# Optimization experiments

Measured on AMD Instinct MI355X. Metric: run time of the kernel, lower is better.

The kernel has to match this reference:

```python
import jax, jax.numpy as jnp
import numpy as np

N, M, E, HID, H = 50000, 4000, 320000, 128, 2
EPS = 1e-5  # torch BatchNorm1d eps


def _lrelu(x):
    return jnp.where(x >= 0, x, 0.2 * x)


def _bn(x, g, b):
    # BatchNorm1d in training mode: biased batch statistics over dim 0
    m = x.mean(0)
    v = ((x - m) ** 2).mean(0)
    return g * (x - m) * jax.lax.rsqrt(v + EPS) + b


def _seg_softmax(a, idx, n):
    # softmax of a[E,heads] normalized per node index idx (PyG softmax)
    mx = jax.ops.segment_max(a, idx, num_segments=n)
    e = jnp.exp(a - mx[idx])
    s = jax.ops.segment_sum(e, idx, num_segments=n)
    return e / s[idx]


def _hgconv(x, he_n, he_e, he_w, W, att, bias, heads):
    # PyG HypergraphConv(use_attention=True, concat=False)
    xl = (x @ W).reshape(N, heads, HID)                  # lin(x) -> [N,heads,C]
    # hyperedge_attr = incidence^T @ x  (matches to_dense_adj path in HGAT)
    ea = jax.ops.segment_sum(x[he_n], he_e, num_segments=M)  # [M,F]
    eal = (ea @ W).reshape(M, heads, HID)                # lin(hyperedge_attr)
    a = (jnp.concatenate([xl[he_n], eal[he_e]], axis=-1) * att[0]).sum(-1)  # [E,heads]
    a = _seg_softmax(_lrelu(a), he_n, N)
    # degree normalizations
    Dn = jax.ops.segment_sum(he_w[he_e], he_n, num_segments=N)
    Dinv = jnp.where(Dn > 0, 1.0 / Dn, 0.0)
    Bn = jax.ops.segment_sum(jnp.ones((E,), x.dtype), he_e, num_segments=M)
    Binv = jnp.where(Bn > 0, 1.0 / Bn, 0.0)
    # node -> hyperedge
    m1 = Binv[he_e][:, None, None] * xl[he_n] * a[..., None]
    eo = jax.ops.segment_sum(m1, he_e, num_segments=M)   # [M,heads,C]
    # hyperedge -> node
    m2 = Dinv[he_n][:, None, None] * eo[he_e] * a[..., None]
    out = jax.ops.segment_sum(m2, he_n, num_segments=N)  # [N,heads,C]
    return out.mean(1) + bias                            # concat=False -> head mean


def _forward(x, he_w, lin1_w, lin1_b, bn1_g, bn1_b, h1_w, h1_att, h1_b,
             bn2_g, bn2_b, h2_w, h2_att, h2_b, bn3_g, bn3_b,
             lin2_w, lin2_b, bn4_g, bn4_b, he_n, he_e):
    src = x
    x = _bn(_lrelu(x @ lin1_w + lin1_b), bn1_g, bn1_b)
    x2 = _hgconv(x, he_n, he_e, he_w, h1_w, h1_att, h1_b, H)
    x = _bn(x + x2, bn2_g, bn2_b)
    x2 = _hgconv(x, he_n, he_e, he_w, h2_w, h2_att, h2_b, 1)
    x = _bn(x + x2, bn3_g, bn3_b)
    x = _lrelu(x @ lin2_w + lin2_b)
    return _bn(src + x, bn4_g, bn4_b)


def setup_inputs() -> dict:
    key = jax.random.key(0)
    ks = jax.random.split(key, 10)
    s = 0.05
    he_n = jax.random.randint(ks[0], (E,), 0, N, dtype=jnp.int32)
    he_e = (jnp.arange(E, dtype=jnp.int32) % M)  # every hyperedge id used
    return {
        'x': jax.random.normal(ks[1], (N, 128), jnp.float32),
        'he_n': he_n, 'he_e': he_e,
        'he_w': jnp.ones((M,), jnp.float32),
        'lin1_w': jax.random.normal(ks[2], (128, HID), jnp.float32) * s,
        'lin1_b': jnp.zeros((HID,), jnp.float32),
        'bn1_g': jnp.ones((HID,), jnp.float32), 'bn1_b': jnp.zeros((HID,), jnp.float32),
        'h1_w': jax.random.normal(ks[3], (HID, H * HID), jnp.float32) * s,
        'h1_att': jax.random.normal(ks[4], (1, H, 2 * HID), jnp.float32) * s,
        'h1_b': jnp.zeros((HID,), jnp.float32),
        'bn2_g': jnp.ones((HID,), jnp.float32), 'bn2_b': jnp.zeros((HID,), jnp.float32),
        'h2_w': jax.random.normal(ks[5], (HID, HID), jnp.float32) * s,
        'h2_att': jax.random.normal(ks[6], (1, 1, 2 * HID), jnp.float32) * s,
        'h2_b': jnp.zeros((HID,), jnp.float32),
        'bn3_g': jnp.ones((HID,), jnp.float32), 'bn3_b': jnp.zeros((HID,), jnp.float32),
        'lin2_w': jax.random.normal(ks[7], (HID, 128), jnp.float32) * s,
        'lin2_b': jnp.zeros((128,), jnp.float32),
        'bn4_g': jnp.ones((128,), jnp.float32), 'bn4_b': jnp.zeros((128,), jnp.float32),
    }


def reference(x, he_n, he_e, he_w, lin1_w, lin1_b, bn1_g, bn1_b, h1_w, h1_att, h1_b,
              bn2_g, bn2_b, h2_w, h2_att, h2_b, bn3_g, bn3_b,
              lin2_w, lin2_b, bn4_g, bn4_b):
    return _forward(x, he_w, lin1_w, lin1_b, bn1_g, bn1_b, h1_w, h1_att, h1_b,
                    bn2_g, bn2_b, h2_w, h2_att, h2_b, bn3_g, bn3_b,
                    lin2_w, lin2_b, bn4_g, bn4_b, he_n, he_e)
```

## Files before the change

### kernel.cpp

```cpp
#include <hip/hip_runtime.h>
#include <hip/hip_fp16.h>
#include <math.h>

constexpr int Nn = 50000;
constexpr int Mm = 4000;
constexpr int Ee = 320000;
constexpr int KPB = Ee / Mm;
constexpr float BINV = 1.0f / (float)KPB;
constexpr float EPSf = 1e-5f;
constexpr int NBKT = 16;
constexpr int NBSCAN = 49;

__device__ __forceinline__ float lrelu_f(float x) { return x >= 0.f ? x : 0.2f * x; }

__device__ __forceinline__ unsigned short f2h(float f) {
    __half h = __float2half_rn(f);
    return *reinterpret_cast<unsigned short*>(&h);
}
__device__ __forceinline__ float h2f(unsigned short s) {
    __half_raw r; r.x = s;
    return __half2float(__half(r));
}
__device__ __forceinline__ unsigned int packh2(float a, float b) {
    return (unsigned int)f2h(a) | ((unsigned int)f2h(b) << 16);
}
__device__ __forceinline__ float4 ldh4(const unsigned short* p) {
    ushort4 u = *(const ushort4*)p;
    return make_float4(h2f(u.x), h2f(u.y), h2f(u.z), h2f(u.w));
}
__device__ __forceinline__ float2 ldh2(const unsigned short* p) {
    ushort2 u = *(const ushort2*)p;
    return make_float2(h2f(u.x), h2f(u.y));
}

__device__ __forceinline__ float wave_sum(float v) {
#pragma unroll
    for (int o = 32; o >= 1; o >>= 1) v += __shfl_xor(v, o, 64);
    return v;
}

__device__ __forceinline__ void finalize_to_lds(const float* __restrict__ st,
                                                const float* __restrict__ g,
                                                const float* __restrict__ b,
                                                float* ABsh, int t) {
    if (t < 128) {
        double ds = 0, dq = 0;
#pragma unroll
        for (int i = 0; i < NBKT; i++) {
            ds += (double)st[i * 256 + t];
            dq += (double)st[i * 256 + 128 + t];
        }
        double mean = ds / (double)Nn;
        double var = dq / (double)Nn - mean * mean;
        float rstd = (float)(1.0 / sqrt(var + (double)EPSf));
        float A = g[t] * rstd;
        ABsh[t] = A;
        ABsh[128 + t] = b[t] - (float)mean * A;
    }
    __syncthreads();
}

__device__ void scan_body(const int* __restrict__ counts, int* __restrict__ offs,
                          int b, int t) {
    __shared__ int sdi[256];
    int pre = 0;
    for (int i = t; i < b * 1024; i += 256) pre += counts[i];
    sdi[t] = pre;
    __syncthreads();
    for (int st = 128; st >= 1; st >>= 1) {
        if (t < st) sdi[t] += sdi[t + st];
        __syncthreads();
    }
    int run0 = sdi[0];
    __syncthreads();
    int c4[4];
    int s = 0;
#pragma unroll
    for (int i = 0; i < 4; i++) {
        int n = b * 1024 + t * 4 + i;
        c4[i] = (n < Nn) ? counts[n] : 0;
        s += c4[i];
    }
    sdi[t] = s;
    __syncthreads();
    for (int off = 1; off < 256; off <<= 1) {
        int v = (t >= off) ? sdi[t - off] : 0;
        __syncthreads();
        sdi[t] += v;
        __syncthreads();
    }
    int run = sdi[t] - s + run0;
#pragma unroll
    for (int i = 0; i < 4; i++) {
        int n = b * 1024 + t * 4 + i;
        if (n < Nn) offs[n] = run;
        run += c4[i];
    }
    if (b == NBSCAN - 1 && t == 255) offs[Nn] = run0 + sdi[255];
}

template <int ROWS, bool LRELU, bool PROBN, bool RESID, bool STATS, bool PACKH2, bool SCANX,
          bool HALFOUT>
__global__ __launch_bounds__(256) void gemmT(const float* __restrict__ A, size_t aystride,
                                             const float* __restrict__ B, int ldb,
                                             const float* __restrict__ bias, float scale,
                                             const float* __restrict__ stIn,
                                             const float* __restrict__ fing,
                                             const float* __restrict__ finb,
                                             const float* __restrict__ resid,
                                             float* __restrict__ stF,
                                             float* __restrict__ C, int ldc, int R,
                                             int gemmBlocksX,
                                             const int* __restrict__ counts,
                                             int* __restrict__ offs) {
    constexpr int RPT = ROWS / 16;
    const int t = threadIdx.x;
    if (SCANX && (int)blockIdx.x >= gemmBlocksX) {
        if (blockIdx.y == 0) scan_body(counts, offs, blockIdx.x - gemmBlocksX, t);
        return;
    }
    __shared__ float As[16][ROWS + 4];
    __shared__ float Bs[16][128];
    __shared__ float Sred[STATS ? 16 : 1][STATS ? 128 : 1];
    __shared__ float ABsh[PROBN ? 256 : 1];
    const int ty = t >> 4, tx = t & 15;
    const int row0 = blockIdx.x * ROWS;
    const int bcol = blockIdx.y * 128;
    A += (size_t)blockIdx.y * aystride;

    if (PROBN) finalize_to_lds(stIn, fing, finb, ABsh, t);

    float4 acc[RPT][2];
#pragma unroll
    for (int i = 0; i < RPT; i++)
#pragma unroll
        for (int q = 0; q < 2; q++) acc[i][q] = make_float4(0.f, 0.f, 0.f, 0.f);

    for (int k0 = 0; k0 < 128; k0 += 16) {
        if (ROWS == 64) {
            int r = t >> 2, kc = (t & 3) * 4;
            int rr = row0 + r;
            rr = rr < R ? rr : R - 1;
            float4 av = *(const float4*)(A + (size_t)rr * 128 + k0 + kc);
            if (PROBN) {
                float4 sA = *(const float4*)&ABsh[k0 + kc];
                float4 sB = *(const float4*)&ABsh[128 + k0 + kc];
                av.x = av.x * sA.x + sB.x; av.y = av.y * sA.y + sB.y;
                av.z = av.z * sA.z + sB.z; av.w = av.w * sA.w + sB.w;
            }
            As[kc + 0][r] = av.x; As[kc + 1][r] = av.y;
            As[kc + 2][r] = av.z; As[kc + 3][r] = av.w;
        } else {
            int r = t >> 3, kc = (t & 7) * 2;
            int rr = row0 + r;
            rr = rr < R ? rr : R - 1;
            float2 av = *(const float2*)(A + (size_t)rr * 128 + k0 + kc);
            if (PROBN) {
                av.x = av.x * ABsh[k0 + kc] + ABsh[128 + k0 + kc];
                av.y = av.y * ABsh[k0 + kc + 1] + ABsh[128 + k0 + kc + 1];
            }
            As[kc + 0][r] = av.x;
            As[kc + 1][r] = av.y;
        }
        {
            int kk = t >> 5, c4 = (t & 31) * 4;
            float4 bv0 = *(const float4*)(B + (size_t)(k0 + kk) * ldb + bcol + c4);
            float4 bv1 = *(const float4*)(B + (size_t)(k0 + kk + 8) * ldb + bcol + c4);
            *(float4*)&Bs[kk][c4] = bv0;
            *(float4*)&Bs[kk + 8][c4] = bv1;
        }
        __syncthreads();
#pragma unroll
        for (int kk = 0; kk < 16; kk++) {
            float ar[RPT];
            if (RPT == 4) {
                float4 a4 = *(const float4*)&As[kk][ty * 4];
                ar[0] = a4.x; ar[1] = a4.y; ar[2] = a4.z; ar[3] = a4.w;
            } else {
                float2 a2 = *(const float2*)&As[kk][ty * 2];
                ar[0] = a2.x; ar[RPT - 1] = a2.y;
            }
            float4 b0 = *(const float4*)&Bs[kk][4 * tx];
            float4 b1 = *(const float4*)&Bs[kk][64 + 4 * tx];
#pragma unroll
            for (int i = 0; i < RPT; i++) {
                acc[i][0].x = fmaf(ar[i], b0.x, acc[i][0].x);
                acc[i][0].y = fmaf(ar[i], b0.y, acc[i][0].y);
                acc[i][0].z = fmaf(ar[i], b0.z, acc[i][0].z);
                acc[i][0].w = fmaf(ar[i], b0.w, acc[i][0].w);
                acc[i][1].x = fmaf(ar[i], b1.x, acc[i][1].x);
                acc[i][1].y = fmaf(ar[i], b1.y, acc[i][1].y);
                acc[i][1].z = fmaf(ar[i], b1.z, acc[i][1].z);
                acc[i][1].w = fmaf(ar[i], b1.w, acc[i][1].w);
            }
        }
        __syncthreads();
    }

    float4 bv0 = make_float4(0.f, 0.f, 0.f, 0.f), bv1 = bv0;
    if (bias) {
        bv0 = *(const float4*)(bias + bcol + 4 * tx);
        bv1 = *(const float4*)(bias + bcol + 64 + 4 * tx);
    }
    float4 cs0 = make_float4(0.f, 0.f, 0.f, 0.f), cs1 = cs0, cq0 = cs0, cq1 = cs0;
#pragma unroll
    for (int i = 0; i < RPT; i++) {
        int row = row0 + ty * RPT + i;
        if (row >= R) continue;
        float4 v0, v1;
        v0.x = acc[i][0].x * scale + bv0.x; v0.y = acc[i][0].y * scale + bv0.y;
        v0.z = acc[i][0].z * scale + bv0.z; v0.w = acc[i][0].w * scale + bv0.w;
        v1.x = acc[i][1].x * scale + bv1.x; v1.y = acc[i][1].y * scale + bv1.y;
        v1.z = acc[i][1].z * scale + bv1.z; v1.w = acc[i][1].w * scale + bv1.w;
        if (LRELU) {
            v0.x = lrelu_f(v0.x); v0.y = lrelu_f(v0.y); v0.z = lrelu_f(v0.z); v0.w = lrelu_f(v0.w);
            v1.x = lrelu_f(v1.x); v1.y = lrelu_f(v1.y); v1.z = lrelu_f(v1.z); v1.w = lrelu_f(v1.w);
        }
        if (RESID) {
            float4 r0 = *(const float4*)(resid + (size_t)row * 128 + bcol + 4 * tx);
            float4 r1 = *(const float4*)(resid + (size_t)row * 128 + bcol + 64 + 4 * tx);
            v0.x += r0.x; v0.y += r0.y; v0.z += r0.z; v0.w += r0.w;
            v1.x += r1.x; v1.y += r1.y; v1.z += r1.z; v1.w += r1.w;
        }
        if (HALFOUT) {
            unsigned short* Ch = (unsigned short*)C;
            if (PACKH2) {
                int h = blockIdx.y;
                unsigned short* c0 = Ch + (size_t)row * ldc + 8 * tx + 2 * h;
                *(unsigned int*)(c0) = packh2(v0.x, v0.y);
                *(unsigned int*)(c0 + 4) = packh2(v0.z, v0.w);
                unsigned short* c1 = Ch + (size_t)row * ldc + 128 + 8 * tx + 2 * h;
                *(unsigned int*)(c1) = packh2(v1.x, v1.y);
                *(unsigned int*)(c1 + 4) = packh2(v1.z, v1.w);
            } else {
                unsigned short* c0 = Ch + (size_t)row * ldc + bcol + 4 * tx;
                *(unsigned int*)(c0) = packh2(v0.x, v0.y);
                *(unsigned int*)(c0 + 2) = packh2(v0.z, v0.w);
                unsigned short* c1 = Ch + (size_t)row * ldc + bcol + 64 + 4 * tx;
                *(unsigned int*)(c1) = packh2(v1.x, v1.y);
                *(unsigned int*)(c1 + 2) = packh2(v1.z, v1.w);
            }
        } else if (PACKH2) {
            int h = blockIdx.y;
            float* c0 = C + (size_t)row * ldc + 8 * tx + 2 * h;
            *(float2*)(c0) = make_float2(v0.x, v0.y);
            *(float2*)(c0 + 4) = make_float2(v0.z, v0.w);
            float* c1 = C + (size_t)row * ldc + 128 + 8 * tx + 2 * h;
            *(float2*)(c1) = make_float2(v1.x, v1.y);
            *(float2*)(c1 + 4) = make_float2(v1.z, v1.w);
        } else {
            *(float4*)(C + (size_t)row * ldc + bcol + 4 * tx) = v0;
            *(float4*)(C + (size_t)row * ldc + bcol + 64 + 4 * tx) = v1;
        }
        if (STATS) {
            cs0.x += v0.x; cs0.y += v0.y; cs0.z += v0.z; cs0.w += v0.w;
            cs1.x += v1.x; cs1.y += v1.y; cs1.z += v1.z; cs1.w += v1.w;
            cq0.x += v0.x * v0.x; cq0.y += v0.y * v0.y; cq0.z += v0.z * v0.z; cq0.w += v0.w * v0.w;
            cq1.x += v1.x * v1.x; cq1.y += v1.y * v1.y; cq1.z += v1.z * v1.z; cq1.w += v1.w * v1.w;
        }
    }
    if (STATS) {
        int bkt = blockIdx.x & (NBKT - 1);
#pragma unroll
        for (int pass = 0; pass < 2; pass++) {
            *(float4*)&Sred[ty][4 * tx] = pass ? cq0 : cs0;
            *(float4*)&Sred[ty][64 + 4 * tx] = pass ? cq1 : cs1;
            __syncthreads();
            if (t < 128) {
                float tot = 0.f;
#pragma unroll
                for (int r = 0; r < 16; r++) tot += Sred[r][t];
                atomicAdd(&stF[bkt * 256 + pass * 128 + t], tot);
            }
            __syncthreads();
        }
    }
}

__global__ void count_edges_watt(const int* __restrict__ he_n, int* __restrict__ counts,
                                 const float* __restrict__ h1_w, const float* __restrict__ h1_att,
                                 const float* __restrict__ h2_w, const float* __restrict__ h2_att,
                                 float* __restrict__ wnA, float* __restrict__ weA,
                                 int* __restrict__ he_nT) {
    int t = threadIdx.x;
    if (blockIdx.x == 1250) {
        for (int j = 0; j < 3; j++) {
            int id = t + 256 * j;
            if (id >= 768) break;
            int which = id / 384;
            int rem = id % 384;
            int h3 = rem >> 7, k = rem & 127;
            float s = 0.f;
            if (h3 < 2) {
                const float* wrow = h1_w + (size_t)k * 256 + h3 * 128;
                const float* arow = h1_att + h3 * 256 + which * 128;
                for (int c = 0; c < 128; c++) s += wrow[c] * arow[c];
            } else {
                const float* wrow = h2_w + (size_t)k * 128;
                const float* arow = h2_att + which * 128;
                for (int c = 0; c < 128; c++) s += wrow[c] * arow[c];
            }
            (which ? weA : wnA)[h3 * 128 + k] = s;
        }
        return;
    }
    int g = blockIdx.x * 256 + t;
    if (g < Ee) {
        int m = g / KPB;
        int k = g - m * KPB;
        int n = he_n[m + (size_t)k * Mm];
        he_nT[g] = n;
        atomicAdd(&counts[n], 1);
    }
}

template <int H, bool FILL>
__global__ __launch_bounds__(256) void bn_dots(const float* __restrict__ X,
                                               const float* __restrict__ stIn,
                                               const float* __restrict__ fing,
                                               const float* __restrict__ finb,
                                               float* __restrict__ ABout,
                                               const float* __restrict__ wn,
                                               const float* __restrict__ we,
                                               float* __restrict__ an,
                                               float* __restrict__ pe,
                                               unsigned short* __restrict__ bufh,
                                               const int* __restrict__ he_n,
                                               const int* __restrict__ offs,
                                               int* __restrict__ cursor,
                                               int* __restrict__ eid, int mainBlocks) {
    int t = threadIdx.x;
    if (FILL && (int)blockIdx.x >= mainBlocks) {
        int e = (blockIdx.x - mainBlocks) * 256 + t;
        if (e < Ee) {
            int n = he_n[e];
            int p = atomicAdd(&cursor[n], 1);
            eid[offs[n] + p] = e;
        }
        return;
    }
    __shared__ float ABsh[256];
    finalize_to_lds(stIn, fing, finb, ABsh, t);
    if (blockIdx.x == 0) ABout[t] = ABsh[t];
    int w = t >> 6, lane = t & 63;
    float a0 = ABsh[lane], a1 = ABsh[lane + 64];
    float b0 = ABsh[128 + lane], b1 = ABsh[192 + lane];
    float wn0[H], wn1[H], we0[H], we1[H];
#pragma unroll
    for (int h = 0; h < H; h++) {
        wn0[h] = wn[h * 128 + lane]; wn1[h] = wn[h * 128 + 64 + lane];
        we0[h] = we[h * 128 + lane]; we1[h] = we[h * 128 + 64 + lane];
    }
#pragma unroll
    for (int nn = 0; nn < 4; nn++) {
        int row = blockIdx.x * 16 + w * 4 + nn;
        const float* xr = X + (size_t)row * 128;
        float v0 = xr[lane] * a0 + b0;
        float v1 = xr[lane + 64] * a1 + b1;
        bufh[(size_t)row * 128 + lane] = f2h(v0);
        bufh[(size_t)row * 128 + 64 + lane] = f2h(v1);
        float pv[H], qv[H];
#pragma unroll
        for (int h = 0; h < H; h++) {
            pv[h] = wave_sum(v0 * wn0[h] + v1 * wn1[h]);
            qv[h] = wave_sum(v0 * we0[h] + v1 * we1[h]);
        }
        if (lane == 0) {
            if (H == 2) {
                *(float2*)&an[row * 2] = make_float2(pv[0], pv[1]);
                *(float2*)&pe[row * 2] = make_float2(qv[0], qv[1]);
            } else {
                an[row] = pv[0];
                pe[row] = qv[0];
            }
        }
    }
}

__global__ __launch_bounds__(256) void bn_out(const float* __restrict__ X,
                                              const float* __restrict__ stIn,
                                              const float* __restrict__ fing,
                                              const float* __restrict__ finb,
                                              float* __restrict__ Y) {
    __shared__ float ABsh[256];
    int t = threadIdx.x;
    finalize_to_lds(stIn, fing, finb, ABsh, t);
    int w = t >> 6, lane = t & 63;
    float a0 = ABsh[lane], a1 = ABsh[lane + 64];
    float b0 = ABsh[128 + lane], b1 = ABsh[192 + lane];
#pragma unroll
    for (int nn = 0; nn < 4; nn++) {
        int row = blockIdx.x * 16 + w * 4 + nn;
        const float* xr = X + (size_t)row * 128;
        float* yr = Y + (size_t)row * 128;
        yr[lane] = xr[lane] * a0 + b0;
        yr[lane + 64] = xr[lane + 64] * a1 + b1;
    }
}

template <int H>
__global__ __launch_bounds__(256) void ea_from_pe(const int* __restrict__ he_nT,
                                                  const float* __restrict__ pe,
                                                  float* __restrict__ ae) {
    int w = threadIdx.x >> 6, lane = threadIdx.x & 63;
    int m = blockIdx.x * 4 + w;
    if (m >= Mm) return;
    float s[H];
#pragma unroll
    for (int h = 0; h < H; h++) s[h] = 0.f;
    for (int k = lane; k < KPB; k += 64) {
        int idx = he_nT[m * KPB + k];
        if (H == 2) {
            float2 p2 = *(const float2*)(pe + (size_t)idx * 2);
            s[0] += p2.x;
            s[H - 1] += p2.y;
        } else {
            s[0] += pe[idx];
        }
    }
#pragma unroll
    for (int h = 0; h < H; h++) s[h] = wave_sum(s[h]);
    if (lane == 0)
#pragma unroll
        for (int h = 0; h < H; h++) ae[m * H + h] = s[h];
}

template <int H>
__global__ __launch_bounds__(256) void seg_softmax(const int* __restrict__ offs,
                                                   const int* __restrict__ eid,
                                                   const float* __restrict__ an,
                                                   const float* __restrict__ ae,
                                                   const float* __restrict__ he_w,
                                                   float* __restrict__ nsp) {
    int t = threadIdx.x;
    int wv = t >> 6, lane = t & 63;
    int q = lane >> 3, li = lane & 7;
    int n = blockIdx.x * 32 + wv * 8 + q;
    bool valid = n < Nn;
    int base = valid ? offs[n] : 0;
    int deg = valid ? offs[n + 1] - base : 0;
    float anv[H];
#pragma unroll
    for (int h = 0; h < H; h++) anv[h] = valid ? an[n * H + h] : 0.f;

    bool h0 = li < deg, h1 = li + 8 < deg;
    int m0 = 0, m1 = 0;
    float l0[H], l1[H];
    float mx[H];
#pragma unroll
    for (int h = 0; h < H; h++) { mx[h] = -INFINITY; l0[h] = 0.f; l1[h] = 0.f; }
    if (h0) {
        m0 = eid[base + li] % Mm;
#pragma unroll
        for (int h = 0; h < H; h++) {
            l0[h] = lrelu_f(anv[h] + ae[m0 * H + h]);
            mx[h] = fmaxf(mx[h], l0[h]);
        }
    }
    if (h1) {
        m1 = eid[base + li + 8] % Mm;
#pragma unroll
        for (int h = 0; h < H; h++) {
            l1[h] = lrelu_f(anv[h] + ae[m1 * H + h]);
            mx[h] = fmaxf(mx[h], l1[h]);
        }
    }
    for (int c = li + 16; c < deg; c += 8) {
        int m = eid[base + c] % Mm;
#pragma unroll
        for (int h = 0; h < H; h++) mx[h] = fmaxf(mx[h], lrelu_f(anv[h] + ae[m * H + h]));
    }
#pragma unroll
    for (int h = 0; h < H; h++) {
#pragma unroll
        for (int o = 1; o <= 4; o <<= 1) mx[h] = fmaxf(mx[h], __shfl_xor(mx[h], o, 64));
    }
    float sm[H];
#pragma unroll
    for (int h = 0; h < H; h++) sm[h] = 0.f;
    float dn = 0.f;
    if (h0) {
        dn += he_w[m0];
#pragma unroll
        for (int h = 0; h < H; h++) sm[h] += expf(l0[h] - mx[h]);
    }
    if (h1) {
        dn += he_w[m1];
#pragma unroll
        for (int h = 0; h < H; h++) sm[h] += expf(l1[h] - mx[h]);
    }
    for (int c = li + 16; c < deg; c += 8) {
        int m = eid[base + c] % Mm;
        dn += he_w[m];
#pragma unroll
        for (int h = 0; h < H; h++) sm[h] += expf(lrelu_f(anv[h] + ae[m * H + h]) - mx[h]);
    }
#pragma unroll
    for (int o = 1; o <= 4; o <<= 1) dn += __shfl_xor(dn, o, 64);
#pragma unroll
    for (int h = 0; h < H; h++) {
#pragma unroll
        for (int o = 1; o <= 4; o <<= 1) sm[h] += __shfl_xor(sm[h], o, 64);
    }
    if (valid && li == 0) {
        float Dv = dn > 0.f ? 1.0f / dn : 0.0f;
        if (H == 2) {
            *(float4*)(nsp + (size_t)n * 8) = make_float4(anv[0], anv[H - 1], mx[0], mx[H - 1]);
            *(float4*)(nsp + (size_t)n * 8 + 4) =
                make_float4(1.f / sm[0], 1.f / sm[H - 1], 0.5f * Dv, 0.f);
        } else {
            *(float4*)(nsp + (size_t)n * 4) = make_float4(anv[0], mx[0], 1.f / sm[0], Dv);
        }
    }
}

template <int H>
__global__ __launch_bounds__(256) void s_build(const unsigned short* __restrict__ Xh,
                                               const int* __restrict__ he_nT,
                                               const float* __restrict__ nsp,
                                               const float* __restrict__ ae,
                                               float* __restrict__ S) {
    __shared__ int idx[KPB];
    __shared__ float av[KPB][H];
    __shared__ float red[8][H][128];
    int m = blockIdx.x, t = threadIdx.x;
    int g = t >> 5, l = t & 31;
    if (t < KPB) {
        int nd = he_nT[m * KPB + t];
        idx[t] = nd;
        if (H == 2) {
            float4 pa = *(const float4*)(nsp + (size_t)nd * 8);
            float4 pb = *(const float4*)(nsp + (size_t)nd * 8 + 4);
            float2 a2 = *(const float2*)(ae + (size_t)m * 2);
            av[t][0] = expf(lrelu_f(pa.x + a2.x) - pa.z) * pb.x;
            av[t][H - 1] = expf(lrelu_f(pa.y + a2.y) - pa.w) * pb.y;
        } else {
            float4 pa = *(const float4*)(nsp + (size_t)nd * 4);
            float aem = ae[m];
            av[t][0] = expf(lrelu_f(pa.x + aem) - pa.y) * pa.z;
        }
    }
    __syncthreads();
    float4 acc[H];
#pragma unroll
    for (int h = 0; h < H; h++) acc[h] = make_float4(0.f, 0.f, 0.f, 0.f);
#pragma unroll
    for (int kk = 0; kk < KPB / 8; kk++) {
        int k = g + kk * 8;
        ushort4 u = *(const ushort4*)(Xh + (size_t)idx[k] * 128 + l * 4);
        float vx = h2f(u.x), vy = h2f(u.y), vz = h2f(u.z), vw = h2f(u.w);
#pragma unroll
        for (int h = 0; h < H; h++) {
            float a = av[k][h];
            acc[h].x = fmaf(a, vx, acc[h].x);
            acc[h].y = fmaf(a, vy, acc[h].y);
            acc[h].z = fmaf(a, vz, acc[h].z);
            acc[h].w = fmaf(a, vw, acc[h].w);
        }
    }
#pragma unroll
    for (int h = 0; h < H; h++) *(float4*)&red[g][h][l * 4] = acc[h];
    __syncthreads();
    if (t < 32 * H) {
        int h = t >> 5, l2 = t & 31;
        float4 s = make_float4(0.f, 0.f, 0.f, 0.f);
#pragma unroll
        for (int gg = 0; gg < 8; gg++) {
            float4 r = *(const float4*)&red[gg][h][l2 * 4];
            s.x += r.x; s.y += r.y; s.z += r.z; s.w += r.w;
        }
        ((float4*)(S + ((size_t)h * Mm + m) * 128))[l2] = s;
    }
}

template <int H>
__global__ __launch_bounds__(256) void node_agg(const int* __restrict__ offs,
                                                const int* __restrict__ eid,
                                                const float* __restrict__ nsp,
                                                const float* __restrict__ ae,
                                                const unsigned short* __restrict__ eoh,
                                                const float* __restrict__ bias,
                                                const float* __restrict__ AB,
                                                float* __restrict__ stF,
                                                float* __restrict__ T) {
    __shared__ float smem[4][256];
    __shared__ float redS[4][128], redQ[4][128];
    int t = threadIdx.x;
    int w = t >> 6, lane = t & 63;
    int n0 = blockIdx.x * 16 + w * 4;
    int o = offs[n0 + (lane < 4 ? lane : 4)];
    int b0 = __shfl(o, 0, 64);
    int b1 = __shfl(o, 1, 64);
    int b2 = __shfl(o, 2, 64);
    int b3 = __shfl(o, 3, 64);
    int b4 = __shfl(o, 4, 64);
    int cnt = b4 - b0;
    int cnt64 = cnt < 64 ? cnt : 64;

    if (lane < cnt64) {
        int slot = b0 + lane;
        int j = (slot >= b1) + (slot >= b2) + (slot >= b3);
        int e = eid[slot];
        int m = e % Mm;
        if (H == 2) {
            float4 pa = *(const float4*)(nsp + (size_t)(n0 + j) * 8);
            float4 pb = *(const float4*)(nsp + (size_t)(n0 + j) * 8 + 4);
            float2 a2 = *(const float2*)(ae + (size_t)m * 2);
            float c0 = expf(lrelu_f(pa.x + a2.x) - pa.z) * pb.x * pb.z;
            float c1 = expf(lrelu_f(pa.y + a2.y) - pa.w) * pb.y * pb.z;
            *(float4*)&smem[w][4 * lane] = make_float4(__int_as_float(m), c0, c1, 0.f);
        } else {
            float4 pa = *(const float4*)(nsp + (size_t)(n0 + j) * 4);
            float c = expf(lrelu_f(pa.x + ae[m]) - pa.y) * pa.z * pa.w;
            *(float2*)&smem[w][2 * lane] = make_float2(__int_as_float(m), c);
        }
    }
    __syncthreads();

    int s1 = min(b1 - b0, cnt64), s2 = min(b2 - b0, cnt64), s3 = min(b3 - b0, cnt64);
    float2 acc0 = make_float2(0.f, 0.f), acc1 = acc0, acc2 = acc0, acc3 = acc0;

#define NA_BODY(ACC, CBEG, CEND)                                                \
    {                                                                           \
        int c = (CBEG);                                                         \
        for (; c + 1 < (CEND); c += 2) {                                        \
            if (H == 2) {                                                       \
                float4 sa = *(const float4*)&smem[w][4 * c];                    \
                float4 sb = *(const float4*)&smem[w][4 * (c + 1)];              \
                float4 ea = ldh4(eoh + (size_t)__float_as_int(sa.x) * 256 + 4 * lane); \
                float4 eb = ldh4(eoh + (size_t)__float_as_int(sb.x) * 256 + 4 * lane); \
                ACC.x += sa.y * ea.x + sa.z * ea.z + sb.y * eb.x + sb.z * eb.z; \
                ACC.y += sa.y * ea.y + sa.z * ea.w + sb.y * eb.y + sb.z * eb.w; \
            } else {                                                            \
                float2 sa = *(const float2*)&smem[w][2 * c];                    \
                float2 sb = *(const float2*)&smem[w][2 * (c + 1)];              \
                float2 ea = ldh2(eoh + (size_t)__float_as_int(sa.x) * 128 + 2 * lane); \
                float2 eb = ldh2(eoh + (size_t)__float_as_int(sb.x) * 128 + 2 * lane); \
                ACC.x += sa.y * ea.x + sb.y * eb.x;                             \
                ACC.y += sa.y * ea.y + sb.y * eb.y;                             \
            }                                                                   \
        }                                                                       \
        if (c < (CEND)) {                                                       \
            if (H == 2) {                                                       \
                float4 sa = *(const float4*)&smem[w][4 * c];                    \
                float4 ea = ldh4(eoh + (size_t)__float_as_int(sa.x) * 256 + 4 * lane); \
                ACC.x += sa.y * ea.x + sa.z * ea.z;                             \
                ACC.y += sa.y * ea.y + sa.z * ea.w;                             \
            } else {                                                            \
                float2 sa = *(const float2*)&smem[w][2 * c];                    \
                float2 ea = ldh2(eoh + (size_t)__float_as_int(sa.x) * 128 + 2 * lane); \
                ACC.x += sa.y * ea.x;                                           \
                ACC.y += sa.y * ea.y;                                           \
            }                                                                   \
        }                                                                       \
    }
    NA_BODY(acc0, 0, s1)
    NA_BODY(acc1, s1, s2)
    NA_BODY(acc2, s2, s3)
    NA_BODY(acc3, s3, cnt64)
#undef NA_BODY

    for (int ss = 64; ss < cnt; ss++) {
        int slot = b0 + ss;
        int j = (slot >= b1) + (slot >= b2) + (slot >= b3);
        int e = eid[slot];
        int m = e % Mm;
        float cx, cy;
        if (H == 2) {
            float4 pa = *(const float4*)(nsp + (size_t)(n0 + j) * 8);
            float4 pb = *(const float4*)(nsp + (size_t)(n0 + j) * 8 + 4);
            float2 a2 = *(const float2*)(ae + (size_t)m * 2);
            float c0 = expf(lrelu_f(pa.x + a2.x) - pa.z) * pb.x * pb.z;
            float c1 = expf(lrelu_f(pa.y + a2.y) - pa.w) * pb.y * pb.z;
            float4 ev = ldh4(eoh + (size_t)m * 256 + 4 * lane);
            cx = c0 * ev.x + c1 * ev.z;
            cy = c0 * ev.y + c1 * ev.w;
        } else {
            float4 pa = *(const float4*)(nsp + (size_t)(n0 + j) * 4);
            float c = expf(lrelu_f(pa.x + ae[m]) - pa.y) * pa.z * pa.w;
            float2 ev = ldh2(eoh + (size_t)m * 128 + 2 * lane);
            cx = c * ev.x;
            cy = c * ev.y;
        }
        if (j == 0) { acc0.x += cx; acc0.y += cy; }
        else if (j == 1) { acc1.x += cx; acc1.y += cy; }
        else if (j == 2) { acc2.x += cx; acc2.y += cy; }
        else { acc3.x += cx; acc3.y += cy; }
    }

    int col = 2 * lane;
    float2 A2 = *(const float2*)(AB + col);
    float2 B2 = *(const float2*)(AB + 128 + col);
    float2 bi = *(const float2*)(bias + col);
    float cs0 = 0.f, cs1 = 0.f, cq0 = 0.f, cq1 = 0.f;
    float2 accs[4] = {acc0, acc1, acc2, acc3};
#pragma unroll
    for (int j = 0; j < 4; j++) {
        int n = n0 + j;
        float2 xr = *(const float2*)(T + (size_t)n * 128 + col);
        float r0 = xr.x * A2.x + B2.x + bi.x + accs[j].x;
        float r1 = xr.y * A2.y + B2.y + bi.y + accs[j].y;
        *(float2*)(T + (size_t)n * 128 + col) = make_float2(r0, r1);
        cs0 += r0; cs1 += r1;
        cq0 += r0 * r0; cq1 += r1 * r1;
    }
    redS[w][col] = cs0; redS[w][col + 1] = cs1;
    redQ[w][col] = cq0; redQ[w][col + 1] = cq1;
    __syncthreads();
    if (t < 128) {
        float s = 0.f, qq = 0.f;
#pragma unroll
        for (int ww = 0; ww < 4; ww++) { s += redS[ww][t]; qq += redQ[ww][t]; }
        int bkt = blockIdx.x & (NBKT - 1);
        atomicAdd(&stF[bkt * 256 + t], s);
        atomicAdd(&stF[bkt * 256 + 128 + t], qq);
    }
}

extern "C" void kernel_launch(void* const* d_in, const int* in_sizes, int n_in,
                              void* d_out, int out_size, void* d_ws, size_t ws_size,
                              hipStream_t stream) {
    const float* x = (const float*)d_in[0];
    const int* he_n = (const int*)d_in[1];
    const float* he_w = (const float*)d_in[3];
    const float* lin1_w = (const float*)d_in[4];
    const float* lin1_b = (const float*)d_in[5];
    const float* bn1_g = (const float*)d_in[6];
    const float* bn1_b = (const float*)d_in[7];
    const float* h1_w = (const float*)d_in[8];
    const float* h1_att = (const float*)d_in[9];
    const float* h1_b = (const float*)d_in[10];
    const float* bn2_g = (const float*)d_in[11];
    const float* bn2_b = (const float*)d_in[12];
    const float* h2_w = (const float*)d_in[13];
    const float* h2_att = (const float*)d_in[14];
    const float* h2_b = (const float*)d_in[15];
    const float* bn3_g = (const float*)d_in[16];
    const float* bn3_b = (const float*)d_in[17];
    const float* lin2_w = (const float*)d_in[18];
    const float* lin2_b = (const float*)d_in[19];
    const float* bn4_g = (const float*)d_in[20];
    const float* bn4_b = (const float*)d_in[21];
    float* out = (float*)d_out;

    char* ws = (char*)d_ws;
    size_t off = 0;
    auto alloc = [&](size_t bytes) -> char* {
        char* p = ws + off;
        off = (off + bytes + 255) & ~(size_t)255;
        return p;
    };
    int* counts = (int*)alloc((size_t)Nn * 4);
    int* cursor = (int*)alloc((size_t)Nn * 4);
    float* stats = (float*)alloc((size_t)4 * NBKT * 256 * 4);
    size_t zbytes = off;
    int* offs = (int*)alloc((size_t)(Nn + 1) * 4);
    int* eid = (int*)alloc((size_t)Ee * 4);
    int* he_nT = (int*)alloc((size_t)Ee * 4);
    float* an = (float*)alloc((size_t)Nn * 2 * 4);
    float* pe = (float*)alloc((size_t)Nn * 2 * 4);
    float* ae = (float*)alloc((size_t)Mm * 2 * 4);
    float* nsp = (float*)alloc((size_t)Nn * 8 * 4);
    float* S = (float*)alloc((size_t)2 * Mm * 128 * 4);
    unsigned short* eoh = (unsigned short*)alloc((size_t)2 * Mm * 128 * 2);
    float* wnA = (float*)alloc(384 * 4);
    float* weA = (float*)alloc(384 * 4);
    float* AB = (float*)alloc(2 * 256 * 4);
    unsigned short* bufh = (unsigned short*)alloc((size_t)Nn * 128 * 2);
    float* buf = (float*)alloc((size_t)Nn * 128 * 4);

    float* st0 = stats;
    float* st1 = stats + NBKT * 256;
    float* st2 = stats + 2 * NBKT * 256;
    float* st3 = stats + 3 * NBKT * 256;
    float *AB1 = AB, *AB2 = AB + 256;

    hipMemsetAsync(d_ws, 0, zbytes, stream);

    constexpr int GB32 = (Nn + 31) / 32;
    count_edges_watt<<<1251, 256, 0, stream>>>(he_n, counts, h1_w, h1_att, h2_w, h2_att,
                                               wnA, weA, he_nT);

    gemmT<32, true, false, false, true, false, true, false>
        <<<dim3(GB32 + NBSCAN, 1), 256, 0, stream>>>(
        x, 0, lin1_w, 128, lin1_b, 1.f, nullptr, nullptr, nullptr, nullptr, st0, buf, 128, Nn,
        GB32, counts, offs);
    bn_dots<2, true><<<3125 + 1250, 256, 0, stream>>>(buf, st0, bn1_g, bn1_b, AB1, wnA, weA,
                                                      an, pe, bufh, he_n, offs, cursor, eid,
                                                      3125);

    ea_from_pe<2><<<Mm / 4, 256, 0, stream>>>(he_nT, pe, ae);
    seg_softmax<2><<<(Nn + 31) / 32, 256, 0, stream>>>(offs, eid, an, ae, he_w, nsp);
    s_build<2><<<Mm, 256, 0, stream>>>(bufh, he_nT, nsp, ae, S);
    gemmT<32, false, false, false, false, true, false, true><<<dim3(125, 2), 256, 0, stream>>>(
        S, (size_t)Mm * 128, h1_w, 256, nullptr, BINV, nullptr, nullptr, nullptr, nullptr,
        nullptr, (float*)eoh, 256, Mm, 125, nullptr, nullptr);
    node_agg<2><<<3125, 256, 0, stream>>>(offs, eid, nsp, ae, eoh, h1_b, AB1, st1, buf);

    bn_dots<1, false><<<3125, 256, 0, stream>>>(buf, st1, bn2_g, bn2_b, AB2, wnA + 256,
                                                weA + 256, an, pe, bufh, nullptr, nullptr,
                                                nullptr, nullptr, 3125);

    ea_from_pe<1><<<Mm / 4, 256, 0, stream>>>(he_nT, pe, ae);
    seg_softmax<1><<<(Nn + 31) / 32, 256, 0, stream>>>(offs, eid, an, ae, he_w, nsp);
    s_build<1><<<Mm, 256, 0, stream>>>(bufh, he_nT, nsp, ae, S);
    gemmT<32, false, false, false, false, false, false, true><<<dim3(125, 1), 256, 0, stream>>>(
        S, 0, h2_w, 128, nullptr, BINV, nullptr, nullptr, nullptr, nullptr, nullptr,
        (float*)eoh, 128, Mm, 125, nullptr, nullptr);
    node_agg<1><<<3125, 256, 0, stream>>>(offs, eid, nsp, ae, eoh, h2_b, AB2, st2, buf);

    gemmT<32, true, true, true, true, false, false, false><<<dim3(GB32, 1), 256, 0, stream>>>(
        buf, 0, lin2_w, 128, lin2_b, 1.f, st2, bn3_g, bn3_b, x, st3, buf, 128, Nn,
        GB32, nullptr, nullptr);
    bn_out<<<3125, 256, 0, stream>>>(buf, st3, bn4_g, bn4_b, out);
}
```

Baseline: 358.6 us.

## Store node activation buffer in fp16 throughout and apply BN on load

Replaces the fp32 node activation buffer and its separate fp16 copy with a single fp16 buffer. The GEMMs and node_agg write fp16, and bn_dots, s_build, the final GEMM and bn_out read fp16 and apply the batch-norm affine on the fly. bn_dots no longer writes the normalized fp16 copy, and s_build applies the BN scale and shift itself. This cuts global memory traffic on the N×128 activations across many kernels, at the cost of fp16 rounding of pre-BN activations, including the residual path. The final GEMM also reads and writes the same buffer in place.

```diff
diff --git a/kernel.cpp b/kernel.cpp
--- a/kernel.cpp
+++ b/kernel.cpp
@@ -100,7 +100,7 @@
 }
 
 template <int ROWS, bool LRELU, bool PROBN, bool RESID, bool STATS, bool PACKH2, bool SCANX,
-          bool HALFOUT>
+          bool HALFOUT, bool HALFIN>
 __global__ __launch_bounds__(256) void gemmT(const float* __restrict__ A, size_t aystride,
                                              const float* __restrict__ B, int ldb,
                                              const float* __restrict__ bias, float scale,
@@ -154,7 +154,12 @@
             int r = t >> 3, kc = (t & 7) * 2;
             int rr = row0 + r;
             rr = rr < R ? rr : R - 1;
-            float2 av = *(const float2*)(A + (size_t)rr * 128 + k0 + kc);
+            float2 av;
+            if (HALFIN) {
+                av = ldh2((const unsigned short*)A + (size_t)rr * 128 + k0 + kc);
+            } else {
+                av = *(const float2*)(A + (size_t)rr * 128 + k0 + kc);
+            }
             if (PROBN) {
                 av.x = av.x * ABsh[k0 + kc] + ABsh[128 + k0 + kc];
                 av.y = av.y * ABsh[k0 + kc + 1] + ABsh[128 + k0 + kc + 1];
@@ -315,7 +320,7 @@
 }
 
 template <int H, bool FILL>
-__global__ __launch_bounds__(256) void bn_dots(const float* __restrict__ X,
+__global__ __launch_bounds__(256) void bn_dots(const unsigned short* __restrict__ X,
                                                const float* __restrict__ stIn,
                                                const float* __restrict__ fing,
                                                const float* __restrict__ finb,
@@ -324,7 +329,6 @@
                                                const float* __restrict__ we,
                                                float* __restrict__ an,
                                                float* __restrict__ pe,
-                                               unsigned short* __restrict__ bufh,
                                                const int* __restrict__ he_n,
                                                const int* __restrict__ offs,
                                                int* __restrict__ cursor,
@@ -354,11 +358,9 @@
 #pragma unroll
     for (int nn = 0; nn < 4; nn++) {
         int row = blockIdx.x * 16 + w * 4 + nn;
-        const float* xr = X + (size_t)row * 128;
-        float v0 = xr[lane] * a0 + b0;
-        float v1 = xr[lane + 64] * a1 + b1;
-        bufh[(size_t)row * 128 + lane] = f2h(v0);
-        bufh[(size_t)row * 128 + 64 + lane] = f2h(v1);
+        const unsigned short* xr = X + (size_t)row * 128;
+        float v0 = h2f(xr[lane]) * a0 + b0;
+        float v1 = h2f(xr[lane + 64]) * a1 + b1;
         float pv[H], qv[H];
 #pragma unroll
         for (int h = 0; h < H; h++) {
@@ -377,7 +379,7 @@
     }
 }
 
-__global__ __launch_bounds__(256) void bn_out(const float* __restrict__ X,
+__global__ __launch_bounds__(256) void bn_out(const unsigned short* __restrict__ X,
                                               const float* __restrict__ stIn,
                                               const float* __restrict__ fing,
                                               const float* __restrict__ finb,
@@ -391,10 +393,10 @@
 #pragma unroll
     for (int nn = 0; nn < 4; nn++) {
         int row = blockIdx.x * 16 + w * 4 + nn;
-        const float* xr = X + (size_t)row * 128;
+        const unsigned short* xr = X + (size_t)row * 128;
         float* yr = Y + (size_t)row * 128;
-        yr[lane] = xr[lane] * a0 + b0;
-        yr[lane + 64] = xr[lane + 64] * a1 + b1;
+        yr[lane] = h2f(xr[lane]) * a0 + b0;
+        yr[lane + 64] = h2f(xr[lane + 64]) * a1 + b1;
     }
 }
 
@@ -516,6 +518,7 @@
 
 template <int H>
 __global__ __launch_bounds__(256) void s_build(const unsigned short* __restrict__ Xh,
+                                               const float* __restrict__ AB,
                                                const int* __restrict__ he_nT,
                                                const float* __restrict__ nsp,
                                                const float* __restrict__ ae,
@@ -541,21 +544,26 @@
         }
     }
     __syncthreads();
+    float4 A4 = ((const float4*)AB)[l];
+    float4 B4 = ((const float4*)(AB + 128))[l];
     float4 acc[H];
 #pragma unroll
     for (int h = 0; h < H; h++) acc[h] = make_float4(0.f, 0.f, 0.f, 0.f);
 #pragma unroll
     for (int kk = 0; kk < KPB / 8; kk++) {
         int k = g + kk * 8;
-        ushort4 u = *(const ushort4*)(Xh + (size_t)idx[k] * 128 + l * 4);
-        float vx = h2f(u.x), vy = h2f(u.y), vz = h2f(u.z), vw = h2f(u.w);
+        float4 v = ldh4(Xh + (size_t)idx[k] * 128 + l * 4);
+        v.x = v.x * A4.x + B4.x;
+        v.y = v.y * A4.y + B4.y;
+        v.z = v.z * A4.z + B4.z;
+        v.w = v.w * A4.w + B4.w;
 #pragma unroll
         for (int h = 0; h < H; h++) {
             float a = av[k][h];
-            acc[h].x = fmaf(a, vx, acc[h].x);
-            acc[h].y = fmaf(a, vy, acc[h].y);
-            acc[h].z = fmaf(a, vz, acc[h].z);
-            acc[h].w = fmaf(a, vw, acc[h].w);
+            acc[h].x = fmaf(a, v.x, acc[h].x);
+            acc[h].y = fmaf(a, v.y, acc[h].y);
+            acc[h].z = fmaf(a, v.z, acc[h].z);
+            acc[h].w = fmaf(a, v.w, acc[h].w);
         }
     }
 #pragma unroll
@@ -582,7 +590,7 @@
                                                 const float* __restrict__ bias,
                                                 const float* __restrict__ AB,
                                                 float* __restrict__ stF,
-                                                float* __restrict__ T) {
+                                                unsigned short* __restrict__ T) {
     __shared__ float smem[4][256];
     __shared__ float redS[4][128], redQ[4][128];
     int t = threadIdx.x;
@@ -697,10 +705,10 @@
 #pragma unroll
     for (int j = 0; j < 4; j++) {
         int n = n0 + j;
-        float2 xr = *(const float2*)(T + (size_t)n * 128 + col);
+        float2 xr = ldh2(T + (size_t)n * 128 + col);
         float r0 = xr.x * A2.x + B2.x + bi.x + accs[j].x;
         float r1 = xr.y * A2.y + B2.y + bi.y + accs[j].y;
-        *(float2*)(T + (size_t)n * 128 + col) = make_float2(r0, r1);
+        *(unsigned int*)(T + (size_t)n * 128 + col) = packh2(r0, r1);
         cs0 += r0; cs1 += r1;
         cq0 += r0 * r0; cq1 += r1 * r1;
     }
@@ -766,8 +774,7 @@
     float* wnA = (float*)alloc(384 * 4);
     float* weA = (float*)alloc(384 * 4);
     float* AB = (float*)alloc(2 * 256 * 4);
-    unsigned short* bufh = (unsigned short*)alloc((size_t)Nn * 128 * 2);
-    float* buf = (float*)alloc((size_t)Nn * 128 * 4);
+    unsigned short* bufq = (unsigned short*)alloc((size_t)Nn * 128 * 2);
 
     float* st0 = stats;
     float* st1 = stats + NBKT * 256;
@@ -781,36 +788,38 @@
     count_edges_watt<<<1251, 256, 0, stream>>>(he_n, counts, h1_w, h1_att, h2_w, h2_att,
                                                wnA, weA, he_nT);
 
-    gemmT<32, true, false, false, true, false, true, false>
+    gemmT<32, true, false, false, true, false, true, true, false>
         <<<dim3(GB32 + NBSCAN, 1), 256, 0, stream>>>(
-        x, 0, lin1_w, 128, lin1_b, 1.f, nullptr, nullptr, nullptr, nullptr, st0, buf, 128, Nn,
-        GB32, counts, offs);
-    bn_dots<2, true><<<3125 + 1250, 256, 0, stream>>>(buf, st0, bn1_g, bn1_b, AB1, wnA, weA,
-                                                      an, pe, bufh, he_n, offs, cursor, eid,
-                                                      3125);
+        x, 0, lin1_w, 128, lin1_b, 1.f, nullptr, nullptr, nullptr, nullptr, st0,
+        (float*)bufq, 128, Nn, GB32, counts, offs);
+    bn_dots<2, true><<<3125 + 1250, 256, 0, stream>>>(bufq, st0, bn1_g, bn1_b, AB1, wnA, weA,
+                                                      an, pe, he_n, offs, cursor, eid, 3125);
 
     ea_from_pe<2><<<Mm / 4, 256, 0, stream>>>(he_nT, pe, ae);
     seg_softmax<2><<<(Nn + 31) / 32, 256, 0, stream>>>(offs, eid, an, ae, he_w, nsp);
-    s_build<2><<<Mm, 256, 0, stream>>>(bufh, he_nT, nsp, ae, S);
-    gemmT<32, false, false, false, false, true, false, true><<<dim3(125, 2), 256, 0, stream>>>(
+    s_build<2><<<Mm, 256, 0, stream>>>(bufq, AB1, he_nT, nsp, ae, S);
+    gemmT<32, false, false, false, false, true, false, true, false>
+        <<<dim3(125, 2), 256, 0, stream>>>(
         S, (size_t)Mm * 128, h1_w, 256, nullptr, BINV, nullptr, nullptr, nullptr, nullptr,
         nullptr, (float*)eoh, 256, Mm, 125, nullptr, nullptr);
-    node_agg<2><<<3125, 256, 0, stream>>>(offs, eid, nsp, ae, eoh, h1_b, AB1, st1, buf);
-
-    bn_dots<1, false><<<3125, 256, 0, stream>>>(buf, st1, bn2_g, bn2_b, AB2, wnA + 256,
-                                                weA + 256, an, pe, bufh, nullptr, nullptr,
-                                                nullptr, nullptr, 3125);
+    node_agg<2><<<3125, 256, 0, stream>>>(offs, eid, nsp, ae, eoh, h1_b, AB1, st1, bufq);
+
+    bn_dots<1, false><<<3125, 256, 0, stream>>>(bufq, st1, bn2_g, bn2_b, AB2, wnA + 256,
+                                                weA + 256, an, pe, nullptr, nullptr, nullptr,
+                                                nullptr, 3125);
 
     ea_from_pe<1><<<Mm / 4, 256, 0, stream>>>(he_nT, pe, ae);
     seg_softmax<1><<<(Nn + 31) / 32, 256, 0, stream>>>(offs, eid, an, ae, he_w, nsp);
-    s_build<1><<<Mm, 256, 0, stream>>>(bufh, he_nT, nsp, ae, S);
-    gemmT<32, false, false, false, false, false, false, true><<<dim3(125, 1), 256, 0, stream>>>(
+    s_build<1><<<Mm, 256, 0, stream>>>(bufq, AB2, he_nT, nsp, ae, S);
+    gemmT<32, false, false, false, false, false, false, true, false>
+        <<<dim3(125, 1), 256, 0, stream>>>(
         S, 0, h2_w, 128, nullptr, BINV, nullptr, nullptr, nullptr, nullptr, nullptr,
         (float*)eoh, 128, Mm, 125, nullptr, nullptr);
-    node_agg<1><<<3125, 256, 0, stream>>>(offs, eid, nsp, ae, eoh, h2_b, AB2, st2, buf);
-
-    gemmT<32, true, true, true, true, false, false, false><<<dim3(GB32, 1), 256, 0, stream>>>(
-        buf, 0, lin2_w, 128, lin2_b, 1.f, st2, bn3_g, bn3_b, x, st3, buf, 128, Nn,
-        GB32, nullptr, nullptr);
-    bn_out<<<3125, 256, 0, stream>>>(buf, st3, bn4_g, bn4_b, out);
-}
+    node_agg<1><<<3125, 256, 0, stream>>>(offs, eid, nsp, ae, eoh, h2_b, AB2, st2, bufq);
+
+    gemmT<32, true, true, true, true, false, false, true, true>
+        <<<dim3(GB32, 1), 256, 0, stream>>>(
+        (const float*)bufq, 0, lin2_w, 128, lin2_b, 1.f, st2, bn3_g, bn3_b, x, st3,
+        (float*)bufq, 128, Nn, GB32, nullptr, nullptr);
+    bn_out<<<3125, 256, 0, stream>>>(bufq, st3, bn4_g, bn4_b, out);
+}
```

After: 353.7 us. Within noise of the previous version (-1.4%).
